# Performance work log

Hardware: AMD Instinct MI355X
Metric: run time of the kernel (lower is better)

Reference implementation:

```python
import jax, jax.numpy as jnp
import numpy as np

T, B, X, H = 512, 32, 1024, 1024


def setup_inputs() -> dict:
    key = jax.random.key(0)
    ks = jax.random.split(key, 12)
    n = lambda k, s: 0.1 * jax.random.normal(k, s, dtype=jnp.float32)
    return {
        "x": jax.random.normal(ks[0], (T, B, X), dtype=jnp.float32),
        "W_ix": n(ks[1], (X, H)), "W_ih": n(ks[2], (H, H)), "W_ic": n(ks[3], (H, H)),
        "W_fx": n(ks[4], (X, H)), "W_fh": n(ks[5], (H, H)), "W_fc": n(ks[6], (H, H)),
        "W_cx": n(ks[7], (X, H)), "W_ch": n(ks[8], (H, H)),
        "W_ox": n(ks[9], (X, H)), "W_oh": n(ks[10], (H, H)), "W_oc": n(ks[11], (H, H)),
        "b_i": jnp.zeros((H,), jnp.float32),
        "b_f": jnp.zeros((B, H), jnp.float32),  # faithful: per-batch forget bias
        "b_c": jnp.zeros((H,), jnp.float32),
        "b_o": jnp.zeros((H,), jnp.float32),
    }


def reference(x, W_ix, W_ih, W_ic, W_fx, W_fh, W_fc, W_cx, W_ch,
              W_ox, W_oh, W_oc, b_i, b_f, b_c, b_o):
    Bv, Hv = x.shape[1], W_ih.shape[0]

    # Precompute all input-side projections in one batched GEMM pass: [T,B,4H]
    Wx = jnp.concatenate([W_ix, W_fx, W_cx, W_ox], axis=1)
    xg = jnp.einsum('tbx,xg->tbg', x, Wx)
    xi, xf, xc, xo = jnp.split(xg, 4, axis=-1)

    def step(carry, xs):
        h_1, c_1 = carry
        xi_t, xf_t, xc_t, xo_t = xs
        i = jax.nn.sigmoid(xi_t + h_1 @ W_ih + c_1 @ W_ic + b_i)
        f = jax.nn.sigmoid(xf_t + h_1 @ W_fh + c_1 @ W_fc + b_f)
        c = f * c_1 + i * jnp.tanh(xc_t + h_1 @ W_ch + b_c)
        o = jax.nn.sigmoid(xo_t + h_1 @ W_oh + c @ W_oc + b_o)
        h = o * jnp.tanh(c)
        return (h, c), None

    h0 = jnp.zeros((Bv, Hv), x.dtype)
    c0 = jnp.zeros((Bv, Hv), x.dtype)
    (h, c), _ = jax.lax.scan(step, (h0, c0), (xi, xf, xc, xo))
    return h
```

## Files before the change

kernel.cpp:

```cpp
#include <hip/hip_runtime.h>
#include <hip/hip_bf16.h>
#include <stdint.h>

typedef unsigned short u16;
typedef uint32_t u32;
typedef unsigned long long u64;
typedef float f32x4 __attribute__((ext_vector_type(4)));
typedef __bf16 bf16x8 __attribute__((ext_vector_type(8)));

__device__ inline u16 f2bf(float f) {
  __bf16 h = (__bf16)f;
  return __builtin_bit_cast(u16, h);
}
__device__ inline float bf2f(u16 u) {
  u32 x = ((u32)u) << 16;
  return __builtin_bit_cast(float, x);
}
__device__ inline f32x4 mfma16(bf16x8 a, bf16x8 b, f32x4 c) {
  return __builtin_amdgcn_mfma_f32_16x16x32_bf16(a, b, c, 0, 0, 0);
}
__device__ inline void cvt8(const float* p, bf16x8& h, bf16x8& l) {
  f32x4 u = *(const f32x4*)p;
  f32x4 v = *(const f32x4*)(p + 4);
#pragma unroll
  for (int i = 0; i < 4; ++i) {
    float a = u[i]; __bf16 ah = (__bf16)a; h[i] = ah; l[i] = (__bf16)(a - (float)ah);
    float b = v[i]; __bf16 bh = (__bf16)b; h[i + 4] = bh; l[i + 4] = (__bf16)(b - (float)bh);
  }
}
__device__ inline void gather8(const float* p, bf16x8& h, bf16x8& l) {
#pragma unroll
  for (int e = 0; e < 8; ++e) {
    float f = p[(size_t)e * 1024];
    __bf16 x = (__bf16)f;
    h[e] = x; l[e] = (__bf16)(f - (float)x);
  }
}

__device__ inline u64 ld64(const u64* p) {
  return __hip_atomic_load(p, __ATOMIC_RELAXED, __HIP_MEMORY_SCOPE_AGENT);
}
__device__ inline u32 ld32(const u32* p) {
  return __hip_atomic_load(p, __ATOMIC_RELAXED, __HIP_MEMORY_SCOPE_AGENT);
}
__device__ inline void st32(u32* p, u32 v) {
  __hip_atomic_store(p, v, __ATOMIC_RELAXED, __HIP_MEMORY_SCOPE_AGENT);
}

struct B16Pair { u64 a, b; };
__device__ inline bf16x8 ldfrag(const u64* base, int j8, int row) {
  B16Pair p;
  p.a = ld64(base + (j8 << 6) + row);
  p.b = ld64(base + (j8 << 6) + 32 + row);
  return __builtin_bit_cast(bf16x8, p);
}

struct RecArgs {
  const float* x;
  const float *W_ix, *W_ih, *W_ic, *W_fx, *W_fh, *W_fc, *W_cx, *W_ch;
  const float *W_ox, *W_oh, *W_oc;
  const float *b_i, *b_f, *b_c, *b_o;
  u32 *hB, *cB;
  u32* flags;
  u32* done;
  float* out;
};

__device__ inline void gbar(u32* flags, u32* done, unsigned ep, int wg) {
  __syncthreads();
  const int tid = threadIdx.x;
  if (tid == 0) st32(flags + wg, ep);
  if (wg == 0) {
    const int wv = tid >> 6, ln = tid & 63;
    if (wv < 4) {
      int it = 0;
      for (;;) {
        u32 v = ld32(flags + wv * 64 + ln);
        if (__ballot(v >= ep) == ~0ull) break;
        if (++it > 400000) break;
        __builtin_amdgcn_s_sleep(1);
      }
    }
    __syncthreads();
    if (tid == 0) st32(done, ep);
  }
  if (tid == 0) {
    int it = 0;
    while (ld32(done) < ep && it < 400000) {
      __builtin_amdgcn_s_sleep(1);
      ++it;
    }
  }
  __syncthreads();
}

__global__ __launch_bounds__(512, 2) void lstm_rec(RecArgs a) {
  __shared__ float scr[8 * 2 * 16 * 16];

  const int tid = threadIdx.x;
  const int wg = blockIdx.x;
  const int j0 = wg * 4;
  const int lane = tid & 63;
  const int wave = tid >> 6;
  const int mrow = lane & 15;
  const int kgroup = lane >> 4;
  const int kq = kgroup * 8;
  const int kw = wave * 128;
  const int col = lane & 15;
  const int rq = (lane >> 4) * 4;

  const u64* H64 = (const u64*)a.hB;
  const u64* C64 = (const u64*)a.cB;

  const int fjj = col >> 2, fg = col & 3;
  const int fj = j0 + fjj;
  const float* Wx = (fg == 0) ? a.W_ix : (fg == 1) ? a.W_fx : (fg == 2) ? a.W_cx : a.W_ox;
  const float* Wh = (fg == 0) ? a.W_ih : (fg == 1) ? a.W_fh : (fg == 2) ? a.W_ch : a.W_oh;
  const float* Wc = (fg == 0) ? a.W_ic : (fg == 1) ? a.W_fc : (fg == 3) ? a.W_oc : a.W_ic;

  bf16x8 bxh[4], bxl[4], bhh[4], bhl[4], bch[4], bcl[4];
#pragma unroll
  for (int ks = 0; ks < 4; ++ks) {
    const size_t k8 = (size_t)(kw + ks * 32 + kq);
    gather8(Wx + k8 * 1024 + fj, bxh[ks], bxl[ks]);
    gather8(Wh + k8 * 1024 + fj, bhh[ks], bhl[ks]);
    if (fg != 2) {
      gather8(Wc + k8 * 1024 + fj, bch[ks], bcl[ks]);
    } else {
      bf16x8 z = {};
      bch[ks] = z; bcl[ks] = z;
    }
  }

  const int eb = tid >> 2, ejj = tid & 3, ej = j0 + (tid & 3);
  const u32 swidx = ((u32)(ej >> 3) << 7) | ((u32)((ej >> 2) & 1) << 6)
                  | ((u32)eb << 1) | ((u32)(ej >> 1) & 1);
  if (tid < 128 && (tid & 1) == 0) {
    st32(a.hB + swidx, 0u);
    st32(a.cB + swidx, 0u);
  }
  float bi = 0.f, bfv = 0.f, bcv = 0.f, bo = 0.f;
  if (tid < 128) {
    bi = a.b_i[ej]; bfv = a.b_f[eb * 1024 + ej]; bcv = a.b_c[ej]; bo = a.b_o[ej];
  }
  unsigned ep = 0;
  gbar(a.flags, a.done, ++ep, wg);

  float c_reg = 0.f, o_pre = 0.f;
  bf16x8 cf0[4] = {}, cf1[4] = {};

  for (int t = 0; t < 512; ++t) {
    f32x4 acc0 = {}, acc1 = {}, pc0 = {}, pc1 = {};
#pragma unroll
    for (int ks = 0; ks < 4; ++ks) {
      const int ka = kw + ks * 32 + kq;
      const int j8 = wave * 16 + ks * 4 + kgroup;
      bf16x8 ah0 = ldfrag(H64, j8, mrow);
      bf16x8 ah1 = ldfrag(H64, j8, mrow + 16);
      bf16x8 xh0, xl0, xh1, xl1;
      const float* xp = a.x + ((size_t)(t * 32 + mrow) << 10) + ka;
      cvt8(xp, xh0, xl0);
      cvt8(xp + (16 << 10), xh1, xl1);
      acc0 = mfma16(xh0, bxh[ks], acc0);
      acc0 = mfma16(xl0, bxh[ks], acc0);
      acc0 = mfma16(xh0, bxl[ks], acc0);
      acc0 = mfma16(ah0, bhh[ks], acc0);
      acc0 = mfma16(ah0, bhl[ks], acc0);
      pc0  = mfma16(cf0[ks], bch[ks], pc0);
      pc0  = mfma16(cf0[ks], bcl[ks], pc0);
      acc1 = mfma16(xh1, bxh[ks], acc1);
      acc1 = mfma16(xl1, bxh[ks], acc1);
      acc1 = mfma16(xh1, bxl[ks], acc1);
      acc1 = mfma16(ah1, bhh[ks], acc1);
      acc1 = mfma16(ah1, bhl[ks], acc1);
      pc1  = mfma16(cf1[ks], bch[ks], pc1);
      pc1  = mfma16(cf1[ks], bcl[ks], pc1);
    }
    {
      const bool take_pc = (col & 3) != 3;
#pragma unroll
      for (int v = 0; v < 4; ++v) {
        scr[((wave * 2 + 0) * 16 + rq + v) * 16 + col] = acc0[v] + (take_pc ? pc0[v] : 0.f);
        scr[((wave * 2 + 1) * 16 + rq + v) * 16 + col] = acc1[v] + (take_pc ? pc1[v] : 0.f);
      }
    }
    __syncthreads();
    if (tid < 128) {
      float pre[4];
#pragma unroll
      for (int g = 0; g < 4; ++g) {
        float s = 0.f;
#pragma unroll
        for (int w = 0; w < 8; ++w)
          s += scr[((w * 2 + (eb >> 4)) * 16 + (eb & 15)) * 16 + ejj * 4 + g];
        pre[g] = s;
      }
      float iv = 1.f / (1.f + expf(-(pre[0] + bi)));
      float fv = 1.f / (1.f + expf(-(pre[1] + bfv)));
      float cv = tanhf(pre[2] + bcv);
      c_reg = fv * c_reg + iv * cv;
      u32 cb = (u32)f2bf(c_reg);
      u32 cpart = __shfl_xor(cb, 1);
      if ((tid & 1) == 0) st32(a.cB + swidx, cb | (cpart << 16));
      o_pre = pre[3] + bo;
    }
    gbar(a.flags, a.done, ++ep, wg);

    f32x4 a20 = {}, a21 = {};
#pragma unroll
    for (int ks = 0; ks < 4; ++ks) {
      const int j8 = wave * 16 + ks * 4 + kgroup;
      cf0[ks] = ldfrag(C64, j8, mrow);
      cf1[ks] = ldfrag(C64, j8, mrow + 16);
      a20 = mfma16(cf0[ks], bch[ks], a20);
      a20 = mfma16(cf0[ks], bcl[ks], a20);
      a21 = mfma16(cf1[ks], bch[ks], a21);
      a21 = mfma16(cf1[ks], bcl[ks], a21);
    }
#pragma unroll
    for (int v = 0; v < 4; ++v) {
      scr[((wave * 2 + 0) * 16 + rq + v) * 16 + col] = a20[v];
      scr[((wave * 2 + 1) * 16 + rq + v) * 16 + col] = a21[v];
    }
    __syncthreads();
    if (tid < 128) {
      float s = o_pre;
#pragma unroll
      for (int w = 0; w < 8; ++w)
        s += scr[((w * 2 + (eb >> 4)) * 16 + (eb & 15)) * 16 + ejj * 4 + 3];
      float ov = 1.f / (1.f + expf(-s));
      float hv = ov * tanhf(c_reg);
      u32 hb = (u32)f2bf(hv);
      u32 hpart = __shfl_xor(hb, 1);
      if ((tid & 1) == 0) st32(a.hB + swidx, hb | (hpart << 16));
      if (t == 511) a.out[eb * 1024 + ej] = hv;
    }
    gbar(a.flags, a.done, ++ep, wg);
  }
}

extern "C" void kernel_launch(void* const* d_in, const int* in_sizes, int n_in,
                              void* d_out, int out_size, void* d_ws, size_t ws_size,
                              hipStream_t stream) {
  (void)in_sizes; (void)n_in; (void)out_size;
  RecArgs ra;
  ra.x    = (const float*)d_in[0];
  ra.W_ix = (const float*)d_in[1];
  ra.W_ih = (const float*)d_in[2];
  ra.W_ic = (const float*)d_in[3];
  ra.W_fx = (const float*)d_in[4];
  ra.W_fh = (const float*)d_in[5];
  ra.W_fc = (const float*)d_in[6];
  ra.W_cx = (const float*)d_in[7];
  ra.W_ch = (const float*)d_in[8];
  ra.W_ox = (const float*)d_in[9];
  ra.W_oh = (const float*)d_in[10];
  ra.W_oc = (const float*)d_in[11];
  ra.b_i  = (const float*)d_in[12];
  ra.b_f  = (const float*)d_in[13];
  ra.b_c  = (const float*)d_in[14];
  ra.b_o  = (const float*)d_in[15];

  char* ws = (char*)d_ws;
  size_t off = 0;
  auto alloc = [&](size_t bytes) {
    char* p = ws + off;
    off = (off + bytes + 255) & ~(size_t)255;
    return p;
  };
  ra.hB    = (u32*)alloc(32 * 1024 * 2);
  ra.cB    = (u32*)alloc(32 * 1024 * 2);
  ra.flags = (u32*)alloc(1024);
  ra.done  = (u32*)alloc(256);
  ra.out   = (float*)d_out;
  if (off > ws_size) return;

  (void)hipMemsetAsync(ra.flags, 0, 1024, stream);
  (void)hipMemsetAsync(ra.done, 0, 256, stream);

  void* args[] = {&ra};
  hipError_t e = hipLaunchCooperativeKernel((void*)lstm_rec, dim3(256), dim3(512),
                                            args, 0, stream);
  if (e != hipSuccess) {
    lstm_rec<<<dim3(256), dim3(512), 0, stream>>>(ra);
  }
}
```

Baseline: 5.122 ms.

## Split grid barrier into arrive/wait and overlap x prefetch and c-projection

The grid barrier is split into an arrive phase and a wait phase so independent work runs while waiting for other workgroups. The next timestep's x rows are loaded and split to bf16 hi/lo during the first barrier, and the c@W contribution for the next step is computed during the second barrier, taking both off the critical path. The shared scratch row stride is padded to 17 to avoid LDS bank conflicts, and launch bounds are relaxed to one block per CU, which allows more registers for the held prefetch fragments.

```diff
diff --git a/kernel.cpp b/kernel.cpp
--- a/kernel.cpp
+++ b/kernel.cpp
@@ -11,10 +11,6 @@
 __device__ inline u16 f2bf(float f) {
   __bf16 h = (__bf16)f;
   return __builtin_bit_cast(u16, h);
-}
-__device__ inline float bf2f(u16 u) {
-  u32 x = ((u32)u) << 16;
-  return __builtin_bit_cast(float, x);
 }
 __device__ inline f32x4 mfma16(bf16x8 a, bf16x8 b, f32x4 c) {
   return __builtin_amdgcn_mfma_f32_16x16x32_bf16(a, b, c, 0, 0, 0);
@@ -66,10 +62,12 @@
   float* out;
 };
 
-__device__ inline void gbar(u32* flags, u32* done, unsigned ep, int wg) {
+__device__ inline void arriveT(u32* flags, unsigned ep, int wg) {
   __syncthreads();
+  if (threadIdx.x == 0) st32(flags + wg, ep);
+}
+__device__ inline void waitT(u32* flags, u32* done, unsigned ep, int wg) {
   const int tid = threadIdx.x;
-  if (tid == 0) st32(flags + wg, ep);
   if (wg == 0) {
     const int wv = tid >> 6, ln = tid & 63;
     if (wv < 4) {
@@ -94,8 +92,8 @@
   __syncthreads();
 }
 
-__global__ __launch_bounds__(512, 2) void lstm_rec(RecArgs a) {
-  __shared__ float scr[8 * 2 * 16 * 16];
+__global__ __launch_bounds__(512, 1) void lstm_rec(RecArgs a) {
+  __shared__ float scr[8 * 2 * 16 * 17];
 
   const int tid = threadIdx.x;
   const int wg = blockIdx.x;
@@ -143,45 +141,53 @@
   if (tid < 128) {
     bi = a.b_i[ej]; bfv = a.b_f[eb * 1024 + ej]; bcv = a.b_c[ej]; bo = a.b_o[ej];
   }
+
   unsigned ep = 0;
-  gbar(a.flags, a.done, ++ep, wg);
+  arriveT(a.flags, ++ep, wg);
+  bf16x8 xph0[4], xpl0[4], xph1[4], xpl1[4];
+#pragma unroll
+  for (int ks = 0; ks < 4; ++ks) {
+    const float* xp = a.x + ((size_t)mrow << 10) + kw + ks * 32 + kq;
+    cvt8(xp, xph0[ks], xpl0[ks]);
+    cvt8(xp + (16 << 10), xph1[ks], xpl1[ks]);
+  }
+  waitT(a.flags, a.done, ep, wg);
 
   float c_reg = 0.f, o_pre = 0.f;
   bf16x8 cf0[4] = {}, cf1[4] = {};
+  f32x4 pc0 = {}, pc1 = {};
+#pragma unroll
+  for (int ks = 0; ks < 4; ++ks) {
+    pc0 = mfma16(cf0[ks], bch[ks], pc0);
+    pc0 = mfma16(cf0[ks], bcl[ks], pc0);
+    pc1 = mfma16(cf1[ks], bch[ks], pc1);
+    pc1 = mfma16(cf1[ks], bcl[ks], pc1);
+  }
 
   for (int t = 0; t < 512; ++t) {
-    f32x4 acc0 = {}, acc1 = {}, pc0 = {}, pc1 = {};
+    f32x4 acc0 = {}, acc1 = {};
 #pragma unroll
     for (int ks = 0; ks < 4; ++ks) {
-      const int ka = kw + ks * 32 + kq;
       const int j8 = wave * 16 + ks * 4 + kgroup;
       bf16x8 ah0 = ldfrag(H64, j8, mrow);
       bf16x8 ah1 = ldfrag(H64, j8, mrow + 16);
-      bf16x8 xh0, xl0, xh1, xl1;
-      const float* xp = a.x + ((size_t)(t * 32 + mrow) << 10) + ka;
-      cvt8(xp, xh0, xl0);
-      cvt8(xp + (16 << 10), xh1, xl1);
-      acc0 = mfma16(xh0, bxh[ks], acc0);
-      acc0 = mfma16(xl0, bxh[ks], acc0);
-      acc0 = mfma16(xh0, bxl[ks], acc0);
+      acc0 = mfma16(xph0[ks], bxh[ks], acc0);
+      acc0 = mfma16(xpl0[ks], bxh[ks], acc0);
+      acc0 = mfma16(xph0[ks], bxl[ks], acc0);
       acc0 = mfma16(ah0, bhh[ks], acc0);
       acc0 = mfma16(ah0, bhl[ks], acc0);
-      pc0  = mfma16(cf0[ks], bch[ks], pc0);
-      pc0  = mfma16(cf0[ks], bcl[ks], pc0);
-      acc1 = mfma16(xh1, bxh[ks], acc1);
-      acc1 = mfma16(xl1, bxh[ks], acc1);
-      acc1 = mfma16(xh1, bxl[ks], acc1);
+      acc1 = mfma16(xph1[ks], bxh[ks], acc1);
+      acc1 = mfma16(xpl1[ks], bxh[ks], acc1);
+      acc1 = mfma16(xph1[ks], bxl[ks], acc1);
       acc1 = mfma16(ah1, bhh[ks], acc1);
       acc1 = mfma16(ah1, bhl[ks], acc1);
-      pc1  = mfma16(cf1[ks], bch[ks], pc1);
-      pc1  = mfma16(cf1[ks], bcl[ks], pc1);
     }
     {
       const bool take_pc = (col & 3) != 3;
 #pragma unroll
       for (int v = 0; v < 4; ++v) {
-        scr[((wave * 2 + 0) * 16 + rq + v) * 16 + col] = acc0[v] + (take_pc ? pc0[v] : 0.f);
-        scr[((wave * 2 + 1) * 16 + rq + v) * 16 + col] = acc1[v] + (take_pc ? pc1[v] : 0.f);
+        scr[((wave * 2 + 0) * 16 + rq + v) * 17 + col] = acc0[v] + (take_pc ? pc0[v] : 0.f);
+        scr[((wave * 2 + 1) * 16 + rq + v) * 17 + col] = acc1[v] + (take_pc ? pc1[v] : 0.f);
       }
     }
     __syncthreads();
@@ -192,7 +198,7 @@
         float s = 0.f;
 #pragma unroll
         for (int w = 0; w < 8; ++w)
-          s += scr[((w * 2 + (eb >> 4)) * 16 + (eb & 15)) * 16 + ejj * 4 + g];
+          s += scr[((w * 2 + (eb >> 4)) * 16 + (eb & 15)) * 17 + ejj * 4 + g];
         pre[g] = s;
       }
       float iv = 1.f / (1.f + expf(-(pre[0] + bi)));
@@ -204,7 +210,17 @@
       if ((tid & 1) == 0) st32(a.cB + swidx, cb | (cpart << 16));
       o_pre = pre[3] + bo;
     }
-    gbar(a.flags, a.done, ++ep, wg);
+    arriveT(a.flags, ++ep, wg);
+    {
+      const int tn = (t < 511) ? t + 1 : 511;
+#pragma unroll
+      for (int ks = 0; ks < 4; ++ks) {
+        const float* xp = a.x + ((size_t)(tn * 32 + mrow) << 10) + kw + ks * 32 + kq;
+        cvt8(xp, xph0[ks], xpl0[ks]);
+        cvt8(xp + (16 << 10), xph1[ks], xpl1[ks]);
+      }
+    }
+    waitT(a.flags, a.done, ep, wg);
 
     f32x4 a20 = {}, a21 = {};
 #pragma unroll
@@ -219,15 +235,15 @@
     }
 #pragma unroll
     for (int v = 0; v < 4; ++v) {
-      scr[((wave * 2 + 0) * 16 + rq + v) * 16 + col] = a20[v];
-      scr[((wave * 2 + 1) * 16 + rq + v) * 16 + col] = a21[v];
+      scr[((wave * 2 + 0) * 16 + rq + v) * 17 + col] = a20[v];
+      scr[((wave * 2 + 1) * 16 + rq + v) * 17 + col] = a21[v];
     }
     __syncthreads();
     if (tid < 128) {
       float s = o_pre;
 #pragma unroll
       for (int w = 0; w < 8; ++w)
-        s += scr[((w * 2 + (eb >> 4)) * 16 + (eb & 15)) * 16 + ejj * 4 + 3];
+        s += scr[((w * 2 + (eb >> 4)) * 16 + (eb & 15)) * 17 + ejj * 4 + 3];
       float ov = 1.f / (1.f + expf(-s));
       float hv = ov * tanhf(c_reg);
       u32 hb = (u32)f2bf(hv);
@@ -235,7 +251,19 @@
       if ((tid & 1) == 0) st32(a.hB + swidx, hb | (hpart << 16));
       if (t == 511) a.out[eb * 1024 + ej] = hv;
     }
-    gbar(a.flags, a.done, ++ep, wg);
+    arriveT(a.flags, ++ep, wg);
+    {
+      f32x4 npc0 = {}, npc1 = {};
+#pragma unroll
+      for (int ks = 0; ks < 4; ++ks) {
+        npc0 = mfma16(cf0[ks], bch[ks], npc0);
+        npc0 = mfma16(cf0[ks], bcl[ks], npc0);
+        npc1 = mfma16(cf1[ks], bch[ks], npc1);
+        npc1 = mfma16(cf1[ks], bcl[ks], npc1);
+      }
+      pc0 = npc0; pc1 = npc1;
+    }
+    waitT(a.flags, a.done, ep, wg);
   }
 }
 
```

New measurement: 5.458 ms. 6.6% more time.
